# Performance work log

Measured on AMD Instinct MI355X. Metric: run time of the kernel, lower is better.

The kernel has to match this reference:

```python
import jax, jax.numpy as jnp
import numpy as np

C = 512          # pc_feat_dim == model_channels
NPTS = 5000      # points per sample (hard-coded in source reshape)
BO = 32          # number of samples
P = 20           # parts per sample (all valid)
S = BO * P       # total valid parts / segments = 640
PPP = (BO * NPTS) // S   # points per part = 250
T = BO * NPTS    # total points = 160000
NUM_FREQS = 10


def setup_inputs() -> dict:
    key = jax.random.key(0)
    ks = jax.random.split(key, 16)
    w = lambda k, shp: (jax.random.normal(k, shp, jnp.float32) * 0.02)
    return {
        "noise_param": jax.random.normal(ks[0], (S, 7), jnp.float32),
        "timesteps": jax.random.randint(ks[1], (BO,), 0, 1000, dtype=jnp.int32),
        "part_pcs": jax.random.normal(ks[2], (T, 3), jnp.float32),
        "segment_ids": (jnp.arange(T, dtype=jnp.int32) // PPP),
        "batch_length": jnp.full((S,), PPP, dtype=jnp.int32),
        "pe_w": w(ks[3], (3, C)), "pe_b": jnp.zeros((C,), jnp.float32),
        "t_w1": w(ks[4], (C, C)), "t_b1": jnp.zeros((C,), jnp.float32),
        "t_w2": w(ks[5], (C, C)), "t_b2": jnp.zeros((C,), jnp.float32),
        "pfc_w": w(ks[6], (147, C)), "pfc_b": jnp.zeros((C,), jnp.float32),
        "o_w1": w(ks[7], (C, 256)), "o_b1": jnp.zeros((256,), jnp.float32),
        "bn1_g": jnp.ones((256,), jnp.float32), "bn1_b": jnp.zeros((256,), jnp.float32),
        "o_w2": w(ks[8], (256, 128)), "o_b2": jnp.zeros((128,), jnp.float32),
        "bn2_g": jnp.ones((128,), jnp.float32), "bn2_b": jnp.zeros((128,), jnp.float32),
        "o_w3": w(ks[9], (128, 7)), "o_b3": jnp.zeros((7,), jnp.float32),
    }


def quat_apply(q, p):
    # pytorch3d convention: quaternion real-part-first (w, x, y, z)
    w, v = q[..., :1], q[..., 1:]
    t = 2.0 * jnp.cross(v, p)
    return p + w * t + jnp.cross(v, t)


def timestep_embedding(t, dim):
    half = dim // 2
    freqs = jnp.exp(-jnp.log(10000.0) * jnp.arange(half, dtype=jnp.float32) / half)
    args = t.astype(jnp.float32)[:, None] * freqs[None, :]
    return jnp.concatenate([jnp.cos(args), jnp.sin(args)], axis=-1)


def nerf_embed(x):
    # include_input, log-sampled freqs 2^0..2^9, fns (sin, cos) -> 7*(1+20)=147
    bands = 2.0 ** jnp.arange(NUM_FREQS, dtype=jnp.float32)
    xb = x[:, None, :] * bands[None, :, None]              # [S, F, 7]
    sc = jnp.concatenate([jnp.sin(xb), jnp.cos(xb)], -1)   # [S, F, 14]
    return jnp.concatenate([x, sc.reshape(x.shape[0], -1)], axis=-1)  # [S, 147]


def batchnorm(x, g, b):
    # training-mode BatchNorm1d over batch dim, eps 1e-5 (biased variance)
    m = x.mean(axis=0)
    v = x.var(axis=0)
    return (x - m) * jax.lax.rsqrt(v + 1e-5) * g + b


def reference(noise_param, timesteps, part_pcs, segment_ids, batch_length,
              pe_w, pe_b, t_w1, t_b1, t_w2, t_b2, pfc_w, pfc_b,
              o_w1, o_b1, bn1_g, bn1_b, o_w2, o_b2, bn2_g, bn2_b, o_w3, o_b3):
    # per-part quaternion + translation, applied per-point via gather
    quat = noise_param[:, 3:]
    quat = quat / jnp.linalg.norm(quat, axis=-1, keepdims=True)
    trans = noise_param[:, :3]
    pts = quat_apply(quat[segment_ids], part_pcs) + trans[segment_ids]  # [T, 3]

    # time embedding MLP (Linear -> SiLU -> Linear), per sample
    temb = timestep_embedding(timesteps, C)
    temb = jax.nn.silu(temb @ t_w1 + t_b1) @ t_w2 + t_b2                # [BO, C]

    feats = pts @ pe_w + pe_b                                           # [T, C]
    point_batch = jnp.arange(T, dtype=jnp.int32) // NPTS
    feats = feats + temb[point_batch]

    # per-part param embedding broadcast-added to that part's points
    pemb = nerf_embed(noise_param) @ pfc_w + pfc_b                      # [S, C]
    feats = feats + pemb[segment_ids]

    # (PointTransformer self/cross layers treated as identity)

    # ragged segment mean pooling
    pooled = jax.ops.segment_sum(feats, segment_ids, num_segments=S)
    pooled = pooled / batch_length[:, None].astype(pooled.dtype)        # [S, C]

    # out head (dropout off)
    h = jax.nn.relu(batchnorm(pooled @ o_w1 + o_b1, bn1_g, bn1_b))
    h = jax.nn.relu(batchnorm(h @ o_w2 + o_b2, bn2_g, bn2_b))
    return h @ o_w3 + o_b3                                              # [S, 7]
```

## Files before the change

kernel.cpp:

```cpp
#include <hip/hip_runtime.h>
#include <math.h>

#define NF 147

__global__ __launch_bounds__(256) void kT(
    const int* __restrict__ tsteps,
    const float* __restrict__ t_w1, const float* __restrict__ t_b1,
    const float* __restrict__ t_w2, const float* __restrict__ t_b2,
    const float* __restrict__ pe_w, const float* __restrict__ pe_b,
    const float* __restrict__ pfc_w, const float* __restrict__ pfc_b,
    const float* __restrict__ o_w1,
    float* __restrict__ h1, float* __restrict__ WM,
    int* __restrict__ statsz)
{
    int blk = blockIdx.x, tid = threadIdx.x;

    if (blk < 128) {
        __shared__ float sh[768];
        int b = blk >> 2, jq = blk & 3;
        float* e = sh;
        float* red = sh + 512;
        float tf = (float)tsteps[b];
        float f = expf(-9.210340371976184f * (float)tid * (1.f / 256.f));
        float sn, cs;
        sincosf(tf * f, &sn, &cs);
        e[tid] = cs;
        e[tid + 256] = sn;
        __syncthreads();
        int jj = tid & 127, j = jq * 128 + jj;
        int ks = tid >> 7, k0 = ks << 8;
        float acc = 0.f;
        #pragma unroll 8
        for (int k = k0; k < k0 + 256; k++) acc += e[k] * t_w1[k * 512 + j];
        red[ks * 128 + jj] = acc;
        __syncthreads();
        if (tid < 128) {
            float v = red[tid] + red[128 + tid] + t_b1[jq * 128 + tid];
            h1[b * 512 + jq * 128 + tid] = v / (1.f + expf(-v));
        }
    } else if (blk < 211) {
        __shared__ float srcs[8][512];
        __shared__ float red[4][8][256];
        int m = blk - 128;
        int r8 = m * 8;
        #pragma unroll
        for (int q = 0; q < 4; q++) {
            int idx = tid + q * 256;
            int row = idx >> 7;
            int off4 = (idx & 127) << 2;
            int kr = r8 + row;
            float4 v;
            if (kr < 512)      v = *(const float4*)&t_w2[(size_t)kr * 512 + off4];
            else if (kr < 659) v = *(const float4*)&pfc_w[(size_t)(kr - 512) * 512 + off4];
            else if (kr < 662) v = *(const float4*)&pe_w[(size_t)(kr - 659) * 512 + off4];
            else if (kr == 662) {
                float4 a = *(const float4*)&pe_b[off4];
                float4 bq = *(const float4*)&pfc_b[off4];
                v.x = a.x + bq.x; v.y = a.y + bq.y; v.z = a.z + bq.z; v.w = a.w + bq.w;
            } else             v = *(const float4*)&t_b2[off4];
            *(float4*)&srcs[row][off4] = v;
        }
        __syncthreads();
        int ks = tid >> 6, c4 = (tid & 63) << 2;
        float4 acc[8];
        #pragma unroll
        for (int i = 0; i < 8; i++) acc[i] = make_float4(0.f, 0.f, 0.f, 0.f);
        int j0 = ks * 128;
        #pragma unroll 4
        for (int jj = 0; jj < 128; jj++) {
            int j = j0 + jj;
            float4 w = *(const float4*)&o_w1[j * 256 + c4];
            #pragma unroll
            for (int i = 0; i < 8; i++) {
                float s = srcs[i][j];
                acc[i].x += s * w.x; acc[i].y += s * w.y;
                acc[i].z += s * w.z; acc[i].w += s * w.w;
            }
        }
        #pragma unroll
        for (int i = 0; i < 8; i++) *(float4*)&red[ks][i][c4] = acc[i];
        __syncthreads();
        #pragma unroll
        for (int t = 0; t < 8; t++) {
            int o = tid + t * 256;
            int i = o >> 8, c = o & 255;
            WM[(size_t)(r8 + i) * 256 + c] =
                red[0][i][c] + red[1][i][c] + red[2][i][c] + red[3][i][c];
        }
    } else {
        for (int z = tid; z < 772; z += 256) statsz[z] = 0;
    }
}

__global__ __launch_bounds__(256) void kS(
    const float* __restrict__ noise, const float* __restrict__ pcs,
    const int* __restrict__ bl,
    const float* __restrict__ o_b1,
    const float* __restrict__ h1, const float* __restrict__ WM,
    float* __restrict__ g1, float* __restrict__ tg)
{
    __shared__ float shm[3600];
    __shared__ float np7s[4][8];
    __shared__ float wsum[4][3];
    __shared__ float rms[4][3];
    int blk = blockIdx.x, tid = threadIdx.x;

    if (blk < 160) {
        int s0 = blk * 4;
        {
            const float4* p4 = (const float4*)(pcs + (size_t)blk * 3000);
            #pragma unroll
            for (int i = 0; i < 3; i++) {
                int idx = tid + i * 256;
                if (idx < 750) *(float4*)&shm[idx * 4] = p4[idx];
            }
        }
        if (tid < 28) np7s[tid / 7][tid % 7] = noise[s0 * 7 + tid];
        __syncthreads();
        int w = tid >> 6, lane = tid & 63;
        {
            float sx = 0.f, sy = 0.f, sz = 0.f;
            const float* base = shm + w * 750;
            #pragma unroll
            for (int it = 0; it < 4; it++) {
                int q = lane + it * 64;
                if (q < 250) {
                    sx += base[q * 3 + 0];
                    sy += base[q * 3 + 1];
                    sz += base[q * 3 + 2];
                }
            }
            for (int off = 32; off >= 1; off >>= 1) {
                sx += __shfl_down(sx, off, 64);
                sy += __shfl_down(sy, off, 64);
                sz += __shfl_down(sz, off, 64);
            }
            if (lane == 0) { wsum[w][0] = sx; wsum[w][1] = sy; wsum[w][2] = sz; }
        }
        __syncthreads();
        if (tid < 4) {
            float inv = 1.f / (float)bl[s0 + tid];
            float mx = wsum[tid][0] * inv, my = wsum[tid][1] * inv, mz = wsum[tid][2] * inv;
            float qw = np7s[tid][3], qx = np7s[tid][4], qy = np7s[tid][5], qz = np7s[tid][6];
            float qn = rsqrtf(qw * qw + qx * qx + qy * qy + qz * qz);
            qw *= qn; qx *= qn; qy *= qn; qz *= qn;
            float tx = 2.f * (qy * mz - qz * my);
            float ty = 2.f * (qz * mx - qx * mz);
            float tz = 2.f * (qx * my - qy * mx);
            rms[tid][0] = mx + qw * tx + (qy * tz - qz * ty) + np7s[tid][0];
            rms[tid][1] = my + qw * ty + (qz * tx - qx * tz) + np7s[tid][1];
            rms[tid][2] = mz + qw * tz + (qx * ty - qy * tx) + np7s[tid][2];
        }
        for (int u = tid; u < 4 * NF; u += 256) {
            int r = u / NF, f = u % NF;
            float v;
            if (f < 7) v = np7s[r][f];
            else {
                int j = f - 7;
                int fi = j / 14, x = j % 14;
                float band = (float)(1 << fi);
                v = (x < 7) ? sinf(np7s[r][x] * band) : cosf(np7s[r][x - 7] * band);
            }
            shm[3008 + r * 148 + f] = v;
        }
        __syncthreads();
        int c = tid;
        float b0 = WM[662 * 256 + c];
        float a0 = b0, a1 = b0, a2 = b0, a3 = b0;
        #pragma unroll 7
        for (int f = 0; f < NF; f++) {
            float wv = WM[(512 + f) * 256 + c];
            a0 += shm[3008 + f] * wv;
            a1 += shm[3008 + 148 + f] * wv;
            a2 += shm[3008 + 296 + f] * wv;
            a3 += shm[3008 + 444 + f] * wv;
        }
        #pragma unroll
        for (int d = 0; d < 3; d++) {
            float wv = WM[(659 + d) * 256 + c];
            a0 += rms[0][d] * wv;
            a1 += rms[1][d] * wv;
            a2 += rms[2][d] * wv;
            a3 += rms[3][d] * wv;
        }
        g1[(s0 + 0) * 256 + c] = a0;
        g1[(s0 + 1) * 256 + c] = a1;
        g1[(s0 + 2) * 256 + c] = a2;
        g1[(s0 + 3) * 256 + c] = a3;
    } else {
        int q = blk - 160;
        int b = q >> 1, ch = q & 1;
        float* hrow = shm;
        float* red = shm + 512;
        hrow[tid] = h1[b * 512 + tid];
        hrow[tid + 256] = h1[b * 512 + 256 + tid];
        __syncthreads();
        int cc = tid & 127, c = ch * 128 + cc;
        int ks = tid >> 7, k0 = ks << 8;
        float acc = 0.f;
        #pragma unroll 8
        for (int k = k0; k < k0 + 256; k++) acc += hrow[k] * WM[k * 256 + c];
        red[ks * 128 + cc] = acc;
        __syncthreads();
        if (tid < 128) {
            int c2 = ch * 128 + tid;
            tg[b * 256 + c2] = red[tid] + red[128 + tid] + WM[663 * 256 + c2] + o_b1[c2];
        }
    }
}

__global__ __launch_bounds__(128) void kCD(
    const float* __restrict__ g1, const float* __restrict__ tg,
    float* __restrict__ stats1,
    const float* __restrict__ bn1_g, const float* __restrict__ bn1_b,
    const float* __restrict__ o_w2, const float* __restrict__ o_b2,
    const float* __restrict__ bn2_g, const float* __restrict__ bn2_b,
    const float* __restrict__ o_w3, const float* __restrict__ o_b3,
    float* __restrict__ stats2, int* __restrict__ cntA, int* __restrict__ cntB,
    float* __restrict__ out)
{
    int blk = blockIdx.x, tid = threadIdx.x;
    int r0 = blk * 8;
    __shared__ float rows[8][256];
    __shared__ float scale[256], shift[256];
    __shared__ float rowsB[8][128];
    __shared__ float w3[128 * 7];

    #pragma unroll
    for (int w = 0; w < 4; w++) {
        int idx4 = (tid + w * 128) << 2;
        int r = idx4 >> 8, c = idx4 & 255;
        int s = r0 + r;
        float4 gv = *(const float4*)&g1[s * 256 + c];
        float4 tv = *(const float4*)&tg[(s / 20) * 256 + c];
        gv.x += tv.x; gv.y += tv.y; gv.z += tv.z; gv.w += tv.w;
        *(float4*)&rows[r][c] = gv;
    }
    for (int i = tid; i < 128 * 7; i += 128) w3[i] = o_w3[i];
    __syncthreads();
    for (int c = tid; c < 256; c += 128) {
        float sm = 0.f, ss = 0.f;
        #pragma unroll
        for (int r = 0; r < 8; r++) { float x = rows[r][c]; sm += x; ss += x * x; }
        atomicAdd(&stats1[c], sm);
        atomicAdd(&stats1[256 + c], ss);
    }

    __syncthreads();
    if (tid == 0) {
        __threadfence();
        atomicAdd(cntA, 1);
        while (atomicAdd(cntA, 0) < 80) { }
        __threadfence();
    }
    __syncthreads();

    for (int c = tid; c < 256; c += 128) {
        float m = stats1[c] * (1.f / 640.f);
        float v = stats1[256 + c] * (1.f / 640.f) - m * m;
        float sc = rsqrtf(v + 1e-5f) * bn1_g[c];
        scale[c] = sc;
        shift[c] = bn1_b[c] - m * sc;
    }
    __syncthreads();
    for (int i = tid; i < 2048; i += 128) {
        int r = i >> 8, c = i & 255;
        float x = rows[r][c] * scale[c] + shift[c];
        rows[r][c] = x > 0.f ? x : 0.f;
    }
    __syncthreads();

    float acc[8];
    float bb = o_b2[tid];
    #pragma unroll
    for (int r = 0; r < 8; r++) acc[r] = bb;
    #pragma unroll 8
    for (int k = 0; k < 256; k++) {
        float w = o_w2[k * 128 + tid];
        #pragma unroll
        for (int r = 0; r < 8; r++) acc[r] += rows[r][k] * w;
    }
    float sm = 0.f, ss = 0.f;
    #pragma unroll
    for (int r = 0; r < 8; r++) { sm += acc[r]; ss += acc[r] * acc[r]; }
    atomicAdd(&stats2[tid], sm);
    atomicAdd(&stats2[128 + tid], ss);

    __syncthreads();
    if (tid == 0) {
        __threadfence();
        atomicAdd(cntB, 1);
        while (atomicAdd(cntB, 0) < 80) { }
        __threadfence();
    }
    __syncthreads();

    {
        float m = stats2[tid] * (1.f / 640.f);
        float v = stats2[128 + tid] * (1.f / 640.f) - m * m;
        float sc = rsqrtf(v + 1e-5f) * bn2_g[tid];
        float sh2 = bn2_b[tid] - m * sc;
        #pragma unroll
        for (int r = 0; r < 8; r++) {
            float x = acc[r] * sc + sh2;
            rowsB[r][tid] = x > 0.f ? x : 0.f;
        }
    }
    __syncthreads();
    if (tid < 56) {
        int r = tid / 7, j = tid % 7;
        float a3 = o_b3[j];
        #pragma unroll 8
        for (int k = 0; k < 128; k++) a3 += rowsB[r][k] * w3[k * 7 + j];
        out[(r0 + r) * 7 + j] = a3;
    }
}

extern "C" void kernel_launch(void* const* d_in, const int* in_sizes, int n_in,
                              void* d_out, int out_size, void* d_ws, size_t ws_size,
                              hipStream_t stream) {
    const float* noise = (const float*)d_in[0];
    const int* tsteps = (const int*)d_in[1];
    const float* pcs = (const float*)d_in[2];
    const int* bl = (const int*)d_in[4];
    const float* pe_w = (const float*)d_in[5];
    const float* pe_b = (const float*)d_in[6];
    const float* t_w1 = (const float*)d_in[7];
    const float* t_b1 = (const float*)d_in[8];
    const float* t_w2 = (const float*)d_in[9];
    const float* t_b2 = (const float*)d_in[10];
    const float* pfc_w = (const float*)d_in[11];
    const float* pfc_b = (const float*)d_in[12];
    const float* o_w1 = (const float*)d_in[13];
    const float* o_b1 = (const float*)d_in[14];
    const float* bn1_g = (const float*)d_in[15];
    const float* bn1_b = (const float*)d_in[16];
    const float* o_w2 = (const float*)d_in[17];
    const float* o_b2 = (const float*)d_in[18];
    const float* bn2_g = (const float*)d_in[19];
    const float* bn2_b = (const float*)d_in[20];
    const float* o_w3 = (const float*)d_in[21];
    const float* o_b3 = (const float*)d_in[22];

    float* ws = (float*)d_ws;
    float* h1    = ws + 0;
    float* WM    = ws + 16384;
    float* g1    = ws + 186368;
    float* tg    = ws + 350208;
    float* stats = ws + 358400;
    int*   cnt   = (int*)(ws + 359168);

    kT<<<212, 256, 0, stream>>>(tsteps, t_w1, t_b1, t_w2, t_b2, pe_w, pe_b,
                                pfc_w, pfc_b, o_w1, h1, WM, (int*)stats);
    kS<<<224, 256, 0, stream>>>(noise, pcs, bl, o_b1, h1, WM, g1, tg);
    kCD<<<80, 128, 0, stream>>>(g1, tg, stats, bn1_g, bn1_b, o_w2, o_b2,
                                bn2_g, bn2_b, o_w3, o_b3,
                                stats + 512, cnt, cnt + 1, (float*)d_out);
}
```

Before: 152.3 us.

## Fuse three kernels into one persistent kernel with global grid barriers

Merges the weight-folding, per-segment, and batchnorm head kernels into a single 224-block launch that separates stages with atomic-counter grid barriers, and zeroes the stats and counters with a memset instead of a spare block. The head stage now uses 256 threads and splits the o_w2 reduction over K across two thread halves. The goal is to remove kernel launch gaps and the tail of each launch. In exchange it relies on all 224 blocks being resident at once, and it uses a larger shared-memory footprint for every block.

```diff
diff --git a/kernel.cpp b/kernel.cpp
--- a/kernel.cpp
+++ b/kernel.cpp
@@ -2,47 +2,65 @@
 #include <math.h>
 
 #define NF 147
-
-__global__ __launch_bounds__(256) void kT(
-    const int* __restrict__ tsteps,
+#define NBLK 224
+
+__device__ __forceinline__ void gbar(int* cnt, int target) {
+    __syncthreads();
+    __threadfence();
+    if (threadIdx.x == 0) {
+        atomicAdd(cnt, 1);
+        while (atomicAdd(cnt, 0) < target) { }
+    }
+    __syncthreads();
+    __threadfence();
+}
+
+__global__ __launch_bounds__(256) void kF(
+    const float* __restrict__ noise, const int* __restrict__ tsteps,
+    const float* __restrict__ pcs, const int* __restrict__ bl,
+    const float* __restrict__ pe_w, const float* __restrict__ pe_b,
     const float* __restrict__ t_w1, const float* __restrict__ t_b1,
     const float* __restrict__ t_w2, const float* __restrict__ t_b2,
-    const float* __restrict__ pe_w, const float* __restrict__ pe_b,
     const float* __restrict__ pfc_w, const float* __restrict__ pfc_b,
-    const float* __restrict__ o_w1,
+    const float* __restrict__ o_w1, const float* __restrict__ o_b1,
+    const float* __restrict__ bn1_g, const float* __restrict__ bn1_b,
+    const float* __restrict__ o_w2, const float* __restrict__ o_b2,
+    const float* __restrict__ bn2_g, const float* __restrict__ bn2_b,
+    const float* __restrict__ o_w3, const float* __restrict__ o_b3,
     float* __restrict__ h1, float* __restrict__ WM,
-    int* __restrict__ statsz)
+    float* __restrict__ g1, float* __restrict__ tg,
+    float* __restrict__ stats1, float* __restrict__ stats2,
+    int* __restrict__ cnts, float* __restrict__ out)
 {
+    __shared__ float shm[12288];
+    __shared__ float np7s[4][8];
+    __shared__ float wsum[4][3];
+    __shared__ float rms[4][3];
     int blk = blockIdx.x, tid = threadIdx.x;
 
     if (blk < 128) {
-        __shared__ float sh[768];
         int b = blk >> 2, jq = blk & 3;
-        float* e = sh;
-        float* red = sh + 512;
         float tf = (float)tsteps[b];
         float f = expf(-9.210340371976184f * (float)tid * (1.f / 256.f));
         float sn, cs;
         sincosf(tf * f, &sn, &cs);
-        e[tid] = cs;
-        e[tid + 256] = sn;
+        shm[tid] = cs; shm[256 + tid] = sn;
         __syncthreads();
         int jj = tid & 127, j = jq * 128 + jj;
         int ks = tid >> 7, k0 = ks << 8;
         float acc = 0.f;
         #pragma unroll 8
-        for (int k = k0; k < k0 + 256; k++) acc += e[k] * t_w1[k * 512 + j];
-        red[ks * 128 + jj] = acc;
+        for (int k = k0; k < k0 + 256; k++) acc += shm[k] * t_w1[k * 512 + j];
+        shm[512 + ks * 128 + jj] = acc;
         __syncthreads();
         if (tid < 128) {
-            float v = red[tid] + red[128 + tid] + t_b1[jq * 128 + tid];
+            float v = shm[512 + tid] + shm[640 + tid] + t_b1[jq * 128 + tid];
             h1[b * 512 + jq * 128 + tid] = v / (1.f + expf(-v));
         }
     } else if (blk < 211) {
-        __shared__ float srcs[8][512];
-        __shared__ float red[4][8][256];
-        int m = blk - 128;
-        int r8 = m * 8;
+        int m = blk - 128, r8 = m * 8;
+        float* srcs = shm;
+        float* red  = shm + 4096;
         #pragma unroll
         for (int q = 0; q < 4; q++) {
             int idx = tid + q * 256;
@@ -57,8 +75,8 @@
                 float4 a = *(const float4*)&pe_b[off4];
                 float4 bq = *(const float4*)&pfc_b[off4];
                 v.x = a.x + bq.x; v.y = a.y + bq.y; v.z = a.z + bq.z; v.w = a.w + bq.w;
-            } else             v = *(const float4*)&t_b2[off4];
-            *(float4*)&srcs[row][off4] = v;
+            } else v = *(const float4*)&t_b2[off4];
+            *(float4*)&srcs[row * 512 + off4] = v;
         }
         __syncthreads();
         int ks = tid >> 6, c4 = (tid & 63) << 2;
@@ -72,38 +90,24 @@
             float4 w = *(const float4*)&o_w1[j * 256 + c4];
             #pragma unroll
             for (int i = 0; i < 8; i++) {
-                float s = srcs[i][j];
+                float s = srcs[i * 512 + j];
                 acc[i].x += s * w.x; acc[i].y += s * w.y;
                 acc[i].z += s * w.z; acc[i].w += s * w.w;
             }
         }
         #pragma unroll
-        for (int i = 0; i < 8; i++) *(float4*)&red[ks][i][c4] = acc[i];
+        for (int i = 0; i < 8; i++) *(float4*)&red[(ks * 8 + i) * 256 + c4] = acc[i];
         __syncthreads();
         #pragma unroll
         for (int t = 0; t < 8; t++) {
             int o = tid + t * 256;
             int i = o >> 8, c = o & 255;
-            WM[(size_t)(r8 + i) * 256 + c] =
-                red[0][i][c] + red[1][i][c] + red[2][i][c] + red[3][i][c];
-        }
-    } else {
-        for (int z = tid; z < 772; z += 256) statsz[z] = 0;
-    }
-}
-
-__global__ __launch_bounds__(256) void kS(
-    const float* __restrict__ noise, const float* __restrict__ pcs,
-    const int* __restrict__ bl,
-    const float* __restrict__ o_b1,
-    const float* __restrict__ h1, const float* __restrict__ WM,
-    float* __restrict__ g1, float* __restrict__ tg)
-{
-    __shared__ float shm[3600];
-    __shared__ float np7s[4][8];
-    __shared__ float wsum[4][3];
-    __shared__ float rms[4][3];
-    int blk = blockIdx.x, tid = threadIdx.x;
+            WM[(size_t)(r8 + i) * 256 + c] = red[i * 256 + c] + red[(8 + i) * 256 + c]
+                                           + red[(16 + i) * 256 + c] + red[(24 + i) * 256 + c];
+        }
+    }
+
+    gbar(&cnts[0], NBLK);
 
     if (blk < 160) {
         int s0 = blk * 4;
@@ -190,129 +194,119 @@
     } else {
         int q = blk - 160;
         int b = q >> 1, ch = q & 1;
-        float* hrow = shm;
-        float* red = shm + 512;
-        hrow[tid] = h1[b * 512 + tid];
-        hrow[tid + 256] = h1[b * 512 + 256 + tid];
+        shm[tid] = h1[b * 512 + tid];
+        shm[256 + tid] = h1[b * 512 + 256 + tid];
         __syncthreads();
         int cc = tid & 127, c = ch * 128 + cc;
         int ks = tid >> 7, k0 = ks << 8;
         float acc = 0.f;
         #pragma unroll 8
-        for (int k = k0; k < k0 + 256; k++) acc += hrow[k] * WM[k * 256 + c];
-        red[ks * 128 + cc] = acc;
+        for (int k = k0; k < k0 + 256; k++) acc += shm[k] * WM[k * 256 + c];
+        shm[512 + ks * 128 + cc] = acc;
         __syncthreads();
         if (tid < 128) {
             int c2 = ch * 128 + tid;
-            tg[b * 256 + c2] = red[tid] + red[128 + tid] + WM[663 * 256 + c2] + o_b1[c2];
-        }
-    }
-}
-
-__global__ __launch_bounds__(128) void kCD(
-    const float* __restrict__ g1, const float* __restrict__ tg,
-    float* __restrict__ stats1,
-    const float* __restrict__ bn1_g, const float* __restrict__ bn1_b,
-    const float* __restrict__ o_w2, const float* __restrict__ o_b2,
-    const float* __restrict__ bn2_g, const float* __restrict__ bn2_b,
-    const float* __restrict__ o_w3, const float* __restrict__ o_b3,
-    float* __restrict__ stats2, int* __restrict__ cntA, int* __restrict__ cntB,
-    float* __restrict__ out)
-{
-    int blk = blockIdx.x, tid = threadIdx.x;
+            tg[b * 256 + c2] = shm[512 + tid] + shm[640 + tid] + WM[663 * 256 + c2] + o_b1[c2];
+        }
+    }
+
+    gbar(&cnts[1], NBLK);
+
+    if (blk >= 80) return;
+
     int r0 = blk * 8;
-    __shared__ float rows[8][256];
-    __shared__ float scale[256], shift[256];
-    __shared__ float rowsB[8][128];
-    __shared__ float w3[128 * 7];
+    float* rows  = shm;
+    float* scale = shm + 2048;
+    float* shift = shm + 2304;
+    float* rowsB = shm + 2560;
+    float* w3s   = shm + 3584;
+    float* red2  = shm + 4608;
 
     #pragma unroll
-    for (int w = 0; w < 4; w++) {
-        int idx4 = (tid + w * 128) << 2;
-        int r = idx4 >> 8, c = idx4 & 255;
-        int s = r0 + r;
-        float4 gv = *(const float4*)&g1[s * 256 + c];
-        float4 tv = *(const float4*)&tg[(s / 20) * 256 + c];
+    for (int w = 0; w < 2; w++) {
+        int i4 = tid + w * 256;
+        int r = i4 >> 6, c = (i4 & 63) << 2;
+        float4 gv = *(const float4*)&g1[(size_t)(r0 + r) * 256 + c];
+        float4 tv = *(const float4*)&tg[(size_t)((r0 + r) / 20) * 256 + c];
         gv.x += tv.x; gv.y += tv.y; gv.z += tv.z; gv.w += tv.w;
-        *(float4*)&rows[r][c] = gv;
-    }
-    for (int i = tid; i < 128 * 7; i += 128) w3[i] = o_w3[i];
-    __syncthreads();
-    for (int c = tid; c < 256; c += 128) {
+        *(float4*)&rows[r * 256 + c] = gv;
+    }
+    for (int i = tid; i < 896; i += 256) w3s[i] = o_w3[i];
+    __syncthreads();
+    {
         float sm = 0.f, ss = 0.f;
         #pragma unroll
-        for (int r = 0; r < 8; r++) { float x = rows[r][c]; sm += x; ss += x * x; }
-        atomicAdd(&stats1[c], sm);
-        atomicAdd(&stats1[256 + c], ss);
-    }
-
-    __syncthreads();
-    if (tid == 0) {
-        __threadfence();
-        atomicAdd(cntA, 1);
-        while (atomicAdd(cntA, 0) < 80) { }
-        __threadfence();
-    }
-    __syncthreads();
-
-    for (int c = tid; c < 256; c += 128) {
-        float m = stats1[c] * (1.f / 640.f);
-        float v = stats1[256 + c] * (1.f / 640.f) - m * m;
-        float sc = rsqrtf(v + 1e-5f) * bn1_g[c];
-        scale[c] = sc;
-        shift[c] = bn1_b[c] - m * sc;
-    }
-    __syncthreads();
-    for (int i = tid; i < 2048; i += 128) {
+        for (int r = 0; r < 8; r++) { float x = rows[r * 256 + tid]; sm += x; ss += x * x; }
+        atomicAdd(&stats1[tid], sm);
+        atomicAdd(&stats1[256 + tid], ss);
+    }
+
+    gbar(&cnts[2], 80);
+
+    {
+        float m = stats1[tid] * (1.f / 640.f);
+        float v = stats1[256 + tid] * (1.f / 640.f) - m * m;
+        float sc = rsqrtf(v + 1e-5f) * bn1_g[tid];
+        scale[tid] = sc;
+        shift[tid] = bn1_b[tid] - m * sc;
+    }
+    __syncthreads();
+    for (int i = tid; i < 2048; i += 256) {
         int r = i >> 8, c = i & 255;
-        float x = rows[r][c] * scale[c] + shift[c];
-        rows[r][c] = x > 0.f ? x : 0.f;
-    }
-    __syncthreads();
-
-    float acc[8];
-    float bb = o_b2[tid];
-    #pragma unroll
-    for (int r = 0; r < 8; r++) acc[r] = bb;
-    #pragma unroll 8
-    for (int k = 0; k < 256; k++) {
-        float w = o_w2[k * 128 + tid];
-        #pragma unroll
-        for (int r = 0; r < 8; r++) acc[r] += rows[r][k] * w;
-    }
-    float sm = 0.f, ss = 0.f;
-    #pragma unroll
-    for (int r = 0; r < 8; r++) { sm += acc[r]; ss += acc[r] * acc[r]; }
-    atomicAdd(&stats2[tid], sm);
-    atomicAdd(&stats2[128 + tid], ss);
-
-    __syncthreads();
-    if (tid == 0) {
-        __threadfence();
-        atomicAdd(cntB, 1);
-        while (atomicAdd(cntB, 0) < 80) { }
-        __threadfence();
-    }
-    __syncthreads();
-
+        float x = rows[r * 256 + c] * scale[c] + shift[c];
+        rows[r * 256 + c] = x > 0.f ? x : 0.f;
+    }
+    __syncthreads();
     {
+        int ks = tid >> 7, c2 = tid & 127;
+        float acc[8];
+        #pragma unroll
+        for (int r = 0; r < 8; r++) acc[r] = 0.f;
+        int kb = ks * 128;
+        #pragma unroll 8
+        for (int kk = 0; kk < 128; kk++) {
+            int k = kb + kk;
+            float w = o_w2[k * 128 + c2];
+            #pragma unroll
+            for (int r = 0; r < 8; r++) acc[r] += rows[r * 256 + k] * w;
+        }
+        #pragma unroll
+        for (int r = 0; r < 8; r++) red2[(ks * 8 + r) * 128 + c2] = acc[r];
+    }
+    __syncthreads();
+    if (tid < 128) {
+        float bb = o_b2[tid];
+        float sm = 0.f, ss = 0.f;
+        #pragma unroll
+        for (int r = 0; r < 8; r++) {
+            float h = red2[r * 128 + tid] + red2[(8 + r) * 128 + tid] + bb;
+            rowsB[r * 128 + tid] = h;
+            sm += h; ss += h * h;
+        }
+        atomicAdd(&stats2[tid], sm);
+        atomicAdd(&stats2[128 + tid], ss);
+    }
+
+    gbar(&cnts[3], 80);
+
+    if (tid < 128) {
         float m = stats2[tid] * (1.f / 640.f);
         float v = stats2[128 + tid] * (1.f / 640.f) - m * m;
         float sc = rsqrtf(v + 1e-5f) * bn2_g[tid];
-        float sh2 = bn2_b[tid] - m * sc;
+        float sh = bn2_b[tid] - m * sc;
         #pragma unroll
         for (int r = 0; r < 8; r++) {
-            float x = acc[r] * sc + sh2;
-            rowsB[r][tid] = x > 0.f ? x : 0.f;
+            float x = rowsB[r * 128 + tid] * sc + sh;
+            rowsB[r * 128 + tid] = x > 0.f ? x : 0.f;
         }
     }
     __syncthreads();
     if (tid < 56) {
-        int r = tid / 7, j = tid % 7;
-        float a3 = o_b3[j];
+        int r = tid / 7, jo = tid % 7;
+        float a3 = o_b3[jo];
         #pragma unroll 8
-        for (int k = 0; k < 128; k++) a3 += rowsB[r][k] * w3[k * 7 + j];
-        out[(r0 + r) * 7 + j] = a3;
+        for (int k = 0; k < 128; k++) a3 += rowsB[r * 128 + k] * w3s[k * 7 + jo];
+        out[(r0 + r) * 7 + jo] = a3;
     }
 }
 
@@ -343,17 +337,19 @@
     const float* o_b3 = (const float*)d_in[22];
 
     float* ws = (float*)d_ws;
-    float* h1    = ws + 0;
-    float* WM    = ws + 16384;
-    float* g1    = ws + 186368;
-    float* tg    = ws + 350208;
-    float* stats = ws + 358400;
-    int*   cnt   = (int*)(ws + 359168);
-
-    kT<<<212, 256, 0, stream>>>(tsteps, t_w1, t_b1, t_w2, t_b2, pe_w, pe_b,
-                                pfc_w, pfc_b, o_w1, h1, WM, (int*)stats);
-    kS<<<224, 256, 0, stream>>>(noise, pcs, bl, o_b1, h1, WM, g1, tg);
-    kCD<<<80, 128, 0, stream>>>(g1, tg, stats, bn1_g, bn1_b, o_w2, o_b2,
-                                bn2_g, bn2_b, o_w3, o_b3,
-                                stats + 512, cnt, cnt + 1, (float*)d_out);
+    float* h1     = ws + 0;
+    float* WM     = ws + 16384;
+    float* g1     = ws + 186368;
+    float* tg     = ws + 350208;
+    float* stats1 = ws + 358400;
+    float* stats2 = ws + 358912;
+    int*   cnts   = (int*)(ws + 359168);
+
+    hipMemsetAsync(stats1, 0, (512 + 256 + 8) * sizeof(float), stream);
+    kF<<<NBLK, 256, 0, stream>>>(noise, tsteps, pcs, bl, pe_w, pe_b,
+                                 t_w1, t_b1, t_w2, t_b2, pfc_w, pfc_b,
+                                 o_w1, o_b1, bn1_g, bn1_b, o_w2, o_b2,
+                                 bn2_g, bn2_b, o_w3, o_b3,
+                                 h1, WM, g1, tg, stats1, stats2, cnts,
+                                 (float*)d_out);
 }
```

Result: slower. 237.7 us (+56.1%).

## Move per-part preprocessing into first kernel and split matvec work finer

Applied to the files above, without the earlier changes.

The point-cloud mean, rotation and NeRF embedding work moves from the second kernel into the first. It runs alongside the time-MLP and weight-fold blocks and writes its results to a new global buffer. The weight-fold GEMM now uses 4 rows per block instead of 8, so there are twice as many blocks, and the tg matvec is split into 4 column quarters with a 4-way k reduction. The second kernel then only runs the small projections. This shortens its critical path and fills more CUs, at the cost of an extra global round trip for the embeddings and a larger first launch.

```diff
diff --git a/kernel.cpp b/kernel.cpp
--- a/kernel.cpp
+++ b/kernel.cpp
@@ -2,53 +2,54 @@
 #include <math.h>
 
 #define NF 147
-
-__global__ __launch_bounds__(256) void kT(
-    const int* __restrict__ tsteps,
+#define NBP 152
+
+__global__ __launch_bounds__(256) void k1(
+    const float* __restrict__ noise, const int* __restrict__ tsteps,
+    const float* __restrict__ pcs, const int* __restrict__ bl,
     const float* __restrict__ t_w1, const float* __restrict__ t_b1,
     const float* __restrict__ t_w2, const float* __restrict__ t_b2,
     const float* __restrict__ pe_w, const float* __restrict__ pe_b,
     const float* __restrict__ pfc_w, const float* __restrict__ pfc_b,
     const float* __restrict__ o_w1,
-    float* __restrict__ h1, float* __restrict__ WM,
+    float* __restrict__ h1, float* __restrict__ WM, float* __restrict__ nb,
     int* __restrict__ statsz)
 {
+    __shared__ float shm[6144];
+    __shared__ float np7s[4][8];
+    __shared__ float wsum[4][3];
+    __shared__ float rms[4][3];
     int blk = blockIdx.x, tid = threadIdx.x;
 
     if (blk < 128) {
-        __shared__ float sh[768];
         int b = blk >> 2, jq = blk & 3;
-        float* e = sh;
-        float* red = sh + 512;
         float tf = (float)tsteps[b];
         float f = expf(-9.210340371976184f * (float)tid * (1.f / 256.f));
         float sn, cs;
         sincosf(tf * f, &sn, &cs);
-        e[tid] = cs;
-        e[tid + 256] = sn;
+        shm[tid] = cs; shm[256 + tid] = sn;
         __syncthreads();
         int jj = tid & 127, j = jq * 128 + jj;
         int ks = tid >> 7, k0 = ks << 8;
         float acc = 0.f;
         #pragma unroll 8
-        for (int k = k0; k < k0 + 256; k++) acc += e[k] * t_w1[k * 512 + j];
-        red[ks * 128 + jj] = acc;
+        for (int k = k0; k < k0 + 256; k++) acc += shm[k] * t_w1[k * 512 + j];
+        shm[512 + ks * 128 + jj] = acc;
         __syncthreads();
         if (tid < 128) {
-            float v = red[tid] + red[128 + tid] + t_b1[jq * 128 + tid];
+            float v = shm[512 + tid] + shm[640 + tid] + t_b1[jq * 128 + tid];
             h1[b * 512 + jq * 128 + tid] = v / (1.f + expf(-v));
         }
-    } else if (blk < 211) {
-        __shared__ float srcs[8][512];
-        __shared__ float red[4][8][256];
-        int m = blk - 128;
-        int r8 = m * 8;
-        #pragma unroll
-        for (int q = 0; q < 4; q++) {
+    } else if (blk < 294) {
+        int m = blk - 128, r4 = m * 4;
+        float* srcs = shm;
+        float* red  = shm + 2048;
+        #pragma unroll
+        for (int q = 0; q < 2; q++) {
             int idx = tid + q * 256;
             int row = idx >> 7;
             int off4 = (idx & 127) << 2;
-            int kr = r8 + row;
+            int kr = r4 + row;
             float4 v;
             if (kr < 512)      v = *(const float4*)&t_w2[(size_t)kr * 512 + off4];
             else if (kr < 659) v = *(const float4*)&pfc_w[(size_t)(kr - 512) * 512 + off4];
@@ -57,58 +58,41 @@
                 float4 a = *(const float4*)&pe_b[off4];
                 float4 bq = *(const float4*)&pfc_b[off4];
                 v.x = a.x + bq.x; v.y = a.y + bq.y; v.z = a.z + bq.z; v.w = a.w + bq.w;
-            } else             v = *(const float4*)&t_b2[off4];
-            *(float4*)&srcs[row][off4] = v;
+            } else v = *(const float4*)&t_b2[off4];
+            *(float4*)&srcs[row * 512 + off4] = v;
         }
         __syncthreads();
         int ks = tid >> 6, c4 = (tid & 63) << 2;
-        float4 acc[8];
-        #pragma unroll
-        for (int i = 0; i < 8; i++) acc[i] = make_float4(0.f, 0.f, 0.f, 0.f);
+        float4 acc[4];
+        #pragma unroll
+        for (int i = 0; i < 4; i++) acc[i] = make_float4(0.f, 0.f, 0.f, 0.f);
         int j0 = ks * 128;
         #pragma unroll 4
         for (int jj = 0; jj < 128; jj++) {
             int j = j0 + jj;
             float4 w = *(const float4*)&o_w1[j * 256 + c4];
             #pragma unroll
-            for (int i = 0; i < 8; i++) {
-                float s = srcs[i][j];
+            for (int i = 0; i < 4; i++) {
+                float s = srcs[i * 512 + j];
                 acc[i].x += s * w.x; acc[i].y += s * w.y;
                 acc[i].z += s * w.z; acc[i].w += s * w.w;
             }
         }
         #pragma unroll
-        for (int i = 0; i < 8; i++) *(float4*)&red[ks][i][c4] = acc[i];
-        __syncthreads();
-        #pragma unroll
-        for (int t = 0; t < 8; t++) {
+        for (int i = 0; i < 4; i++) *(float4*)&red[(ks * 4 + i) * 256 + c4] = acc[i];
+        __syncthreads();
+        #pragma unroll
+        for (int t = 0; t < 4; t++) {
             int o = tid + t * 256;
             int i = o >> 8, c = o & 255;
-            WM[(size_t)(r8 + i) * 256 + c] =
-                red[0][i][c] + red[1][i][c] + red[2][i][c] + red[3][i][c];
-        }
-    } else {
-        for (int z = tid; z < 772; z += 256) statsz[z] = 0;
-    }
-}
-
-__global__ __launch_bounds__(256) void kS(
-    const float* __restrict__ noise, const float* __restrict__ pcs,
-    const int* __restrict__ bl,
-    const float* __restrict__ o_b1,
-    const float* __restrict__ h1, const float* __restrict__ WM,
-    float* __restrict__ g1, float* __restrict__ tg)
-{
-    __shared__ float shm[3600];
-    __shared__ float np7s[4][8];
-    __shared__ float wsum[4][3];
-    __shared__ float rms[4][3];
-    int blk = blockIdx.x, tid = threadIdx.x;
-
-    if (blk < 160) {
-        int s0 = blk * 4;
+            WM[(size_t)(r4 + i) * 256 + c] = red[i * 256 + c] + red[(4 + i) * 256 + c]
+                                           + red[(8 + i) * 256 + c] + red[(12 + i) * 256 + c];
+        }
+    } else if (blk < 454) {
+        int blkg = blk - 294;
+        int s0 = blkg * 4;
         {
-            const float4* p4 = (const float4*)(pcs + (size_t)blk * 3000);
+            const float4* p4 = (const float4*)(pcs + (size_t)blkg * 3000);
             #pragma unroll
             for (int i = 0; i < 3; i++) {
                 int idx = tid + i * 256;
@@ -147,9 +131,12 @@
             float tx = 2.f * (qy * mz - qz * my);
             float ty = 2.f * (qz * mx - qx * mz);
             float tz = 2.f * (qx * my - qy * mx);
-            rms[tid][0] = mx + qw * tx + (qy * tz - qz * ty) + np7s[tid][0];
-            rms[tid][1] = my + qw * ty + (qz * tx - qx * tz) + np7s[tid][1];
-            rms[tid][2] = mz + qw * tz + (qx * ty - qy * tx) + np7s[tid][2];
+            float r0 = mx + qw * tx + (qy * tz - qz * ty) + np7s[tid][0];
+            float r1 = my + qw * ty + (qz * tx - qx * tz) + np7s[tid][1];
+            float r2 = mz + qw * tz + (qx * ty - qy * tx) + np7s[tid][2];
+            nb[(size_t)(s0 + tid) * NBP + 148] = r0;
+            nb[(size_t)(s0 + tid) * NBP + 149] = r1;
+            nb[(size_t)(s0 + tid) * NBP + 150] = r2;
         }
         for (int u = tid; u < 4 * NF; u += 256) {
             int r = u / NF, f = u % NF;
@@ -161,7 +148,26 @@
                 float band = (float)(1 << fi);
                 v = (x < 7) ? sinf(np7s[r][x] * band) : cosf(np7s[r][x - 7] * band);
             }
-            shm[3008 + r * 148 + f] = v;
+            nb[(size_t)(s0 + r) * NBP + f] = v;
+        }
+    } else {
+        for (int z = tid; z < 772; z += 256) statsz[z] = 0;
+    }
+}
+
+__global__ __launch_bounds__(256) void k2(
+    const float* __restrict__ o_b1,
+    const float* __restrict__ h1, const float* __restrict__ WM,
+    const float* __restrict__ nb,
+    float* __restrict__ g1, float* __restrict__ tg)
+{
+    __shared__ float shm[1024];
+    int blk = blockIdx.x, tid = threadIdx.x;
+
+    if (blk < 160) {
+        int s0 = blk * 4;
+        if (tid < 152) {
+            ((float4*)shm)[tid] = ((const float4*)(nb + (size_t)s0 * NBP))[tid];
         }
         __syncthreads();
         int c = tid;
@@ -170,18 +176,18 @@
         #pragma unroll 7
         for (int f = 0; f < NF; f++) {
             float wv = WM[(512 + f) * 256 + c];
-            a0 += shm[3008 + f] * wv;
-            a1 += shm[3008 + 148 + f] * wv;
-            a2 += shm[3008 + 296 + f] * wv;
-            a3 += shm[3008 + 444 + f] * wv;
+            a0 += shm[f] * wv;
+            a1 += shm[NBP + f] * wv;
+            a2 += shm[2 * NBP + f] * wv;
+            a3 += shm[3 * NBP + f] * wv;
         }
         #pragma unroll
         for (int d = 0; d < 3; d++) {
             float wv = WM[(659 + d) * 256 + c];
-            a0 += rms[0][d] * wv;
-            a1 += rms[1][d] * wv;
-            a2 += rms[2][d] * wv;
-            a3 += rms[3][d] * wv;
+            a0 += shm[148 + d] * wv;
+            a1 += shm[NBP + 148 + d] * wv;
+            a2 += shm[2 * NBP + 148 + d] * wv;
+            a3 += shm[3 * NBP + 148 + d] * wv;
         }
         g1[(s0 + 0) * 256 + c] = a0;
         g1[(s0 + 1) * 256 + c] = a1;
@@ -189,22 +195,22 @@
         g1[(s0 + 3) * 256 + c] = a3;
     } else {
         int q = blk - 160;
-        int b = q >> 1, ch = q & 1;
-        float* hrow = shm;
-        float* red = shm + 512;
-        hrow[tid] = h1[b * 512 + tid];
-        hrow[tid + 256] = h1[b * 512 + 256 + tid];
-        __syncthreads();
-        int cc = tid & 127, c = ch * 128 + cc;
-        int ks = tid >> 7, k0 = ks << 8;
+        int b = q >> 2, cq = q & 3;
+        shm[tid] = h1[b * 512 + tid];
+        shm[256 + tid] = h1[b * 512 + 256 + tid];
+        __syncthreads();
+        int ks = tid >> 6, cc = tid & 63;
+        int c = cq * 64 + cc;
+        int k0 = ks * 128;
         float acc = 0.f;
         #pragma unroll 8
-        for (int k = k0; k < k0 + 256; k++) acc += hrow[k] * WM[k * 256 + c];
-        red[ks * 128 + cc] = acc;
-        __syncthreads();
-        if (tid < 128) {
-            int c2 = ch * 128 + tid;
-            tg[b * 256 + c2] = red[tid] + red[128 + tid] + WM[663 * 256 + c2] + o_b1[c2];
+        for (int k = k0; k < k0 + 128; k++) acc += shm[k] * WM[k * 256 + c];
+        shm[512 + ks * 64 + cc] = acc;
+        __syncthreads();
+        if (tid < 64) {
+            int c2 = cq * 64 + tid;
+            tg[b * 256 + c2] = shm[512 + tid] + shm[576 + tid] + shm[640 + tid]
+                             + shm[704 + tid] + WM[663 * 256 + c2] + o_b1[c2];
         }
     }
 }
@@ -345,14 +351,16 @@
     float* ws = (float*)d_ws;
     float* h1    = ws + 0;
     float* WM    = ws + 16384;
-    float* g1    = ws + 186368;
-    float* tg    = ws + 350208;
-    float* stats = ws + 358400;
-    int*   cnt   = (int*)(ws + 359168);
-
-    kT<<<212, 256, 0, stream>>>(tsteps, t_w1, t_b1, t_w2, t_b2, pe_w, pe_b,
-                                pfc_w, pfc_b, o_w1, h1, WM, (int*)stats);
-    kS<<<224, 256, 0, stream>>>(noise, pcs, bl, o_b1, h1, WM, g1, tg);
+    float* nb    = ws + 186368;
+    float* g1    = ws + 283648;
+    float* tg    = ws + 447488;
+    float* stats = ws + 455680;
+    int*   cnt   = (int*)(ws + 456448);
+
+    k1<<<455, 256, 0, stream>>>(noise, tsteps, pcs, bl, t_w1, t_b1, t_w2, t_b2,
+                                pe_w, pe_b, pfc_w, pfc_b, o_w1,
+                                h1, WM, nb, (int*)stats);
+    k2<<<288, 256, 0, stream>>>(o_b1, h1, WM, nb, g1, tg);
     kCD<<<80, 128, 0, stream>>>(g1, tg, stats, bn1_g, bn1_b, o_w2, o_b2,
                                 bn2_g, bn2_b, o_w3, o_b3,
                                 stats + 512, cnt, cnt + 1, (float*)d_out);
```

Result: faster. 146.9 us (-3.6%).
